# Kernel optimization log

Measured on AMD Instinct MI355X. Metric: run time of the kernel, lower is better.

The kernel has to match this reference:

```python
import jax, jax.numpy as jnp
import numpy as np

LAMB = 5.0
B, N = 1024, 3125  # batch, anchors (5 anchors x 25x25 map)

def setup_inputs() -> dict:
    key = jax.random.key(0)
    k1, k2, k3, k4 = jax.random.split(key, 4)
    return {
        "c_pred": jax.random.normal(k1, (B, N, 2), dtype=jnp.float32),
        "r_pred": jax.random.normal(k2, (B, N, 4), dtype=jnp.float32),
        "r_target": jax.random.normal(k3, (B, N, 4), dtype=jnp.float32),
        # anchor labels in {-1: ignore, 0: negative, 1: positive}
        "label": jax.random.randint(k4, (B, N), -1, 2, dtype=jnp.int32),
    }

def reference(c_pred, r_pred, r_target, label):
    dt = c_pred.dtype
    pos = (label == 1)
    neg = (label == 0)
    pos_cnt = pos.sum(axis=-1).astype(dt)  # [B]
    neg_cnt = neg.sum(axis=-1).astype(dt)

    # --- classification: masked 2-class cross-entropy, pos/neg balanced per batch ---
    logp = jax.nn.log_softmax(c_pred, axis=-1)  # [B, N, 2]
    ce_pos = -logp[..., 1]                      # CE when target class = 1
    ce_neg = -logp[..., 0]                      # CE when target class = 0
    pos_mean = jnp.where(pos_cnt > 0,
                         (ce_pos * pos).sum(axis=-1) / jnp.maximum(pos_cnt, 1.0), 0.0)
    neg_mean = (ce_neg * neg).sum(axis=-1) / jnp.maximum(neg_cnt, 1.0)
    c_loss = ((pos_mean + neg_mean) * 0.5).mean()

    d = r_pred - r_target
    a = jnp.abs(d)
    sl = jnp.where(a < 1.0, 0.5 * d * d, a - 0.5)  # [B, N, 4]
    # per-batch mean over pos_num*4 elements == masked mean of per-anchor coord-mean
    r_per = (sl.mean(axis=-1) * pos).sum(axis=-1) / jnp.maximum(pos_cnt, 1.0)
    r_loss = jnp.where(pos_cnt > 0, r_per, 0.0).mean()

    t_loss = c_loss + LAMB * r_loss
    return (c_loss, r_loss, t_loss)
```

## Files before the change

kernel.cpp:

```cpp
#include <hip/hip_runtime.h>

#define BATCH 1024
#define NANCH 3125
#define LAMB  5.0f
#define SPLIT 4
#define CHUNK ((NANCH + SPLIT - 1) / SPLIT)
#define NBLK  (BATCH * SPLIT)

__device__ __forceinline__ float wave_red_f(float v) {
    #pragma unroll
    for (int o = 32; o > 0; o >>= 1) v += __shfl_down(v, o, 64);
    return v;
}

__global__ __launch_bounds__(256) void partial_kernel(
    const float* __restrict__ c_pred,
    const float* __restrict__ r_pred,
    const float* __restrict__ r_target,
    const int*   __restrict__ label,
    float*       __restrict__ partial)
{
    const int blk = blockIdx.x;
    const int b   = blk / SPLIT;
    const int s   = blk % SPLIT;
    const int tid = threadIdx.x;

    const float2* c2 = (const float2*)(c_pred   + (size_t)b * NANCH * 2);
    const float4* rp = (const float4*)(r_pred   + (size_t)b * NANCH * 4);
    const float4* rt = (const float4*)(r_target + (size_t)b * NANCH * 4);
    const int*    lb = label + (size_t)b * NANCH;

    const int end = min((s + 1) * CHUNK, NANCH);

    float cp = 0.f, cn = 0.f, sl = 0.f, pc = 0.f, nc = 0.f;

    for (int i = s * CHUNK + tid; i < end; i += 256) {
        const int    l = lb[i];
        const float2 c = c2[i];

        const float m   = fmaxf(c.x, c.y);
        const float lse = m + __logf(1.f + __expf(-fabsf(c.x - c.y)));

        if (l == 1) {
            pc += 1.f;
            cp += lse - c.y;
            const float4 p = rp[i];
            const float4 t = rt[i];
            float s4 = 0.f, d, a;
            d = p.x - t.x; a = fabsf(d); s4 += (a < 1.f) ? 0.5f * d * d : a - 0.5f;
            d = p.y - t.y; a = fabsf(d); s4 += (a < 1.f) ? 0.5f * d * d : a - 0.5f;
            d = p.z - t.z; a = fabsf(d); s4 += (a < 1.f) ? 0.5f * d * d : a - 0.5f;
            d = p.w - t.w; a = fabsf(d); s4 += (a < 1.f) ? 0.5f * d * d : a - 0.5f;
            sl += s4 * 0.25f;
        } else if (l == 0) {
            nc += 1.f;
            cn += lse - c.x;
        }
    }

    cp = wave_red_f(cp);
    cn = wave_red_f(cn);
    sl = wave_red_f(sl);
    pc = wave_red_f(pc);
    nc = wave_red_f(nc);

    __shared__ float sm[5][4];
    const int wid = tid >> 6, lane = tid & 63;
    if (lane == 0) {
        sm[0][wid] = cp; sm[1][wid] = cn; sm[2][wid] = sl;
        sm[3][wid] = pc; sm[4][wid] = nc;
    }
    __syncthreads();
    if (tid < 5) {
        const int k = tid;
        partial[(size_t)blk * 5 + k] = sm[k][0] + sm[k][1] + sm[k][2] + sm[k][3];
    }
}

__global__ __launch_bounds__(512) void finalize_kernel(
    const float* __restrict__ partial,
    float*       __restrict__ out)
{
    const int tid = threadIdx.x;
    float csum = 0.f, rsum = 0.f;

    for (int b = tid; b < BATCH; b += 512) {
        float cp = 0.f, cn = 0.f, sl = 0.f, pc = 0.f, nc = 0.f;
        #pragma unroll
        for (int s = 0; s < SPLIT; ++s) {
            const float* p = partial + ((size_t)b * SPLIT + s) * 5;
            cp += p[0]; cn += p[1]; sl += p[2]; pc += p[3]; nc += p[4];
        }
        const bool haspos = (pc > 0.5f);
        const float pos_mean = haspos ? cp / pc : 0.f;
        const float neg_mean = cn / fmaxf(nc, 1.f);
        csum += (pos_mean + neg_mean) * 0.5f;
        rsum += haspos ? sl / pc : 0.f;
    }

    csum = wave_red_f(csum);
    rsum = wave_red_f(rsum);

    __shared__ float s_c[8], s_r[8];
    const int wid = tid >> 6, lane = tid & 63;
    if (lane == 0) { s_c[wid] = csum; s_r[wid] = rsum; }
    __syncthreads();
    if (tid == 0) {
        float cs = 0.f, rs = 0.f;
        #pragma unroll
        for (int w = 0; w < 8; ++w) { cs += s_c[w]; rs += s_r[w]; }
        const float c_loss = cs / (float)BATCH;
        const float r_loss = rs / (float)BATCH;
        out[0] = c_loss;
        out[1] = r_loss;
        out[2] = c_loss + LAMB * r_loss;
    }
}

extern "C" void kernel_launch(void* const* d_in, const int* in_sizes, int n_in,
                              void* d_out, int out_size, void* d_ws, size_t ws_size,
                              hipStream_t stream) {
    const float* c_pred   = (const float*)d_in[0];
    const float* r_pred   = (const float*)d_in[1];
    const float* r_target = (const float*)d_in[2];
    const int*   label    = (const int*)d_in[3];
    float*       out      = (float*)d_out;
    float*       partial  = (float*)d_ws;

    partial_kernel<<<NBLK, 256, 0, stream>>>(c_pred, r_pred, r_target, label, partial);
    finalize_kernel<<<1, 512, 0, stream>>>(partial, out);
}
```

Before: 29.75 us.

## Process four aligned anchors per thread with vector loads and branchless accumulation

After: 28.25 us. -5.0%, faster.

```diff
diff --git a/kernel.cpp b/kernel.cpp
--- a/kernel.cpp
+++ b/kernel.cpp
@@ -3,14 +3,26 @@
 #define BATCH 1024
 #define NANCH 3125
 #define LAMB  5.0f
-#define SPLIT 4
-#define CHUNK ((NANCH + SPLIT - 1) / SPLIT)
-#define NBLK  (BATCH * SPLIT)
+#define NBLK  (BATCH * 4)
 
 __device__ __forceinline__ float wave_red_f(float v) {
     #pragma unroll
     for (int o = 32; o > 0; o >>= 1) v += __shfl_down(v, o, 64);
     return v;
+}
+
+__device__ __forceinline__ float lse2(float cx, float cy) {
+    const float m = fmaxf(cx, cy);
+    return m + __logf(1.f + __expf(-fabsf(cx - cy)));
+}
+
+__device__ __forceinline__ float sl1(float4 p, float4 t) {
+    float s4 = 0.f, d, a;
+    d = p.x - t.x; a = fabsf(d); s4 += (a < 1.f) ? 0.5f * d * d : a - 0.5f;
+    d = p.y - t.y; a = fabsf(d); s4 += (a < 1.f) ? 0.5f * d * d : a - 0.5f;
+    d = p.z - t.z; a = fabsf(d); s4 += (a < 1.f) ? 0.5f * d * d : a - 0.5f;
+    d = p.w - t.w; a = fabsf(d); s4 += (a < 1.f) ? 0.5f * d * d : a - 0.5f;
+    return s4 * 0.25f;
 }
 
 __global__ __launch_bounds__(256) void partial_kernel(
@@ -21,40 +33,66 @@
     float*       __restrict__ partial)
 {
     const int blk = blockIdx.x;
-    const int b   = blk / SPLIT;
-    const int s   = blk % SPLIT;
+    const int b   = blk >> 2;
+    const int s   = blk & 3;
     const int tid = threadIdx.x;
+    const int u   = (s << 8) | tid;
 
-    const float2* c2 = (const float2*)(c_pred   + (size_t)b * NANCH * 2);
-    const float4* rp = (const float4*)(r_pred   + (size_t)b * NANCH * 4);
-    const float4* rt = (const float4*)(r_target + (size_t)b * NANCH * 4);
-    const int*    lb = label + (size_t)b * NANCH;
+    const int align0  = (4 - (b & 3)) & 3;
+    const int ngroups = (NANCH - align0) >> 2;
+    const int ntail   = NANCH - align0 - (ngroups << 2);
 
-    const int end = min((s + 1) * CHUNK, NANCH);
+    const float*  crow = c_pred + (size_t)b * (NANCH * 2);
+    const float4* rp   = (const float4*)(r_pred   + (size_t)b * NANCH * 4);
+    const float4* rt   = (const float4*)(r_target + (size_t)b * NANCH * 4);
+    const int*    lb   = label + (size_t)b * NANCH;
 
     float cp = 0.f, cn = 0.f, sl = 0.f, pc = 0.f, nc = 0.f;
 
-    for (int i = s * CHUNK + tid; i < end; i += 256) {
-        const int    l = lb[i];
-        const float2 c = c2[i];
+    if (u < ngroups) {
+        const int a = align0 + (u << 2);
 
-        const float m   = fmaxf(c.x, c.y);
-        const float lse = m + __logf(1.f + __expf(-fabsf(c.x - c.y)));
+        const int4   L   = *(const int4*)(lb + a);
+        const float4 C01 = *(const float4*)(crow + 2 * a);
+        const float4 C23 = *(const float4*)(crow + 2 * a + 4);
 
-        if (l == 1) {
-            pc += 1.f;
-            cp += lse - c.y;
-            const float4 p = rp[i];
-            const float4 t = rt[i];
-            float s4 = 0.f, d, a;
-            d = p.x - t.x; a = fabsf(d); s4 += (a < 1.f) ? 0.5f * d * d : a - 0.5f;
-            d = p.y - t.y; a = fabsf(d); s4 += (a < 1.f) ? 0.5f * d * d : a - 0.5f;
-            d = p.z - t.z; a = fabsf(d); s4 += (a < 1.f) ? 0.5f * d * d : a - 0.5f;
-            d = p.w - t.w; a = fabsf(d); s4 += (a < 1.f) ? 0.5f * d * d : a - 0.5f;
-            sl += s4 * 0.25f;
-        } else if (l == 0) {
-            nc += 1.f;
-            cn += lse - c.x;
+        const bool p0 = (L.x == 1), p1 = (L.y == 1), p2 = (L.z == 1), p3 = (L.w == 1);
+        float4 P0, T0, P1, T1, P2, T2, P3, T3;
+        if (p0) { P0 = rp[a];     T0 = rt[a];     }
+        if (p1) { P1 = rp[a + 1]; T1 = rt[a + 1]; }
+        if (p2) { P2 = rp[a + 2]; T2 = rt[a + 2]; }
+        if (p3) { P3 = rp[a + 3]; T3 = rt[a + 3]; }
+
+        const float e0 = lse2(C01.x, C01.y), e1 = lse2(C01.z, C01.w);
+        const float e2 = lse2(C23.x, C23.y), e3 = lse2(C23.z, C23.w);
+        const bool n0 = (L.x == 0), n1 = (L.y == 0), n2 = (L.z == 0), n3 = (L.w == 0);
+
+        pc = (p0 ? 1.f : 0.f) + (p1 ? 1.f : 0.f) + (p2 ? 1.f : 0.f) + (p3 ? 1.f : 0.f);
+        nc = (n0 ? 1.f : 0.f) + (n1 ? 1.f : 0.f) + (n2 ? 1.f : 0.f) + (n3 ? 1.f : 0.f);
+        cp = (p0 ? (e0 - C01.y) : 0.f) + (p1 ? (e1 - C01.w) : 0.f)
+           + (p2 ? (e2 - C23.y) : 0.f) + (p3 ? (e3 - C23.w) : 0.f);
+        cn = (n0 ? (e0 - C01.x) : 0.f) + (n1 ? (e1 - C01.z) : 0.f)
+           + (n2 ? (e2 - C23.x) : 0.f) + (n3 ? (e3 - C23.z) : 0.f);
+
+        if (p0) sl += sl1(P0, T0);
+        if (p1) sl += sl1(P1, T1);
+        if (p2) sl += sl1(P2, T2);
+        if (p3) sl += sl1(P3, T3);
+    } else {
+        const int k = u - ngroups;
+        const int nextra = align0 + ntail;
+        if (k < nextra) {
+            const int a = (k < align0) ? k
+                        : (align0 + (ngroups << 2) + (k - align0));
+            const int   l  = lb[a];
+            const float cx = crow[2 * a], cy = crow[2 * a + 1];
+            const float e  = lse2(cx, cy);
+            if (l == 1) {
+                pc = 1.f; cp = e - cy;
+                sl = sl1(rp[a], rt[a]);
+            } else if (l == 0) {
+                nc = 1.f; cn = e - cx;
+            }
         }
     }
 
@@ -87,8 +125,8 @@
     for (int b = tid; b < BATCH; b += 512) {
         float cp = 0.f, cn = 0.f, sl = 0.f, pc = 0.f, nc = 0.f;
         #pragma unroll
-        for (int s = 0; s < SPLIT; ++s) {
-            const float* p = partial + ((size_t)b * SPLIT + s) * 5;
+        for (int s = 0; s < 4; ++s) {
+            const float* p = partial + ((size_t)b * 4 + s) * 5;
             cp += p[0]; cn += p[1]; sl += p[2]; pc += p[3]; nc += p[4];
         }
         const bool haspos = (pc > 0.5f);
```
